# Kernel tuning notes

Hardware: AMD Instinct MI355X
Metric: run time of the kernel (lower is better)

The kernel has to match this reference:

```python
import jax, jax.numpy as jnp
import numpy as np

D, H1, O, E = 1024, 4096, 1024, 8
B = 8192


def setup_inputs() -> dict:
    key = jax.random.key(0)
    k1, k2, k3, k4 = jax.random.split(key, 4)
    # kaiming_uniform_ with nonlinearity='relu': bound = sqrt(6 / fan_in), fan_in = last dim
    b_w1 = float(np.sqrt(6.0 / D))
    b_w2 = float(np.sqrt(6.0 / H1))
    x = jax.random.normal(k1, (B, D), dtype=jnp.float32)
    eid = jax.random.randint(k2, (B,), 0, E, dtype=jnp.int32)
    W1 = jax.random.uniform(k3, (E, H1, D), dtype=jnp.float32, minval=-b_w1, maxval=b_w1)
    W2 = jax.random.uniform(k4, (E, O, H1), dtype=jnp.float32, minval=-b_w2, maxval=b_w2)
    b2 = jnp.zeros((E, O), dtype=jnp.float32)
    return {"x": x, "eid": eid, "W1": W1, "W2": W2, "b2": b2}


def reference(x, eid, W1, W2, b2):
    # Per-token expert MLP: y_i = gelu(x_i @ W1[eid_i].T) @ W2[eid_i].T + b2[eid_i]
    # Dense-dispatch formulation: loop over the (small, static) expert axis,
    # compute each expert MLP on all tokens, and select per-token via mask.
    # Math is identical to the sort/gather/scatter original.
    y = jnp.zeros((x.shape[0], W2.shape[1]), dtype=x.dtype)
    for e in range(W1.shape[0]):
        h = jax.nn.gelu(x @ W1[e].T, approximate=False)   # [B, H1]
        y_e = h @ W2[e].T + b2[e]                          # [B, O]
        mask = (eid == e)[:, None].astype(x.dtype)
        y = y + mask * y_e
    return y
```

## Files before the change

### kernel.cpp

```cpp
#include <hip/hip_runtime.h>
#include <hip/hip_bf16.h>
#include <math.h>

constexpr int kD  = 1024;
constexpr int kH1 = 4096;
constexpr int kO  = 1024;
constexpr int kE  = 8;
constexpr int kB  = 8192;

constexpr int BM = 128;
constexpr int BN = 128;
constexpr int BK = 32;
constexpr int MAXT = kB / BM + kE;

typedef __attribute__((ext_vector_type(8))) short short8;
typedef __attribute__((ext_vector_type(4))) float f32x4;

__device__ __forceinline__ unsigned short f2bf(float f) {
  unsigned int u = __float_as_uint(f);
  u += 0x7fffu + ((u >> 16) & 1u);
  return (unsigned short)(u >> 16);
}

__device__ __forceinline__ float gelu_exact(float v) {
  return 0.5f * v * (1.0f + erff(v * 0.70710678118654752f));
}

__global__ __launch_bounds__(256) void setup_kernel(const int* __restrict__ eid,
                                                    int* __restrict__ perm,
                                                    int* __restrict__ tiles) {
  __shared__ int cnt[kE];
  __shared__ int off[kE];
  __shared__ int cur[kE];
  int t = threadIdx.x;
  if (t < kE) { cnt[t] = 0; cur[t] = 0; }
  __syncthreads();
  for (int i = t; i < kB; i += 256) atomicAdd(&cnt[eid[i]], 1);
  __syncthreads();
  if (t == 0) {
    int o = 0, nt = 0;
    for (int e = 0; e < kE; ++e) {
      off[e] = o;
      int c = cnt[e];
      for (int r = 0; r < c; r += BM) {
        tiles[nt * 4 + 0] = e;
        tiles[nt * 4 + 1] = o + r;
        tiles[nt * 4 + 2] = (c - r < BM) ? (c - r) : BM;
        tiles[nt * 4 + 3] = 0;
        ++nt;
      }
      o += c;
    }
    for (; nt < MAXT; ++nt) {
      tiles[nt * 4 + 0] = 0; tiles[nt * 4 + 1] = 0;
      tiles[nt * 4 + 2] = 0; tiles[nt * 4 + 3] = 0;
    }
  }
  __syncthreads();
  for (int i = t; i < kB; i += 256) {
    int e = eid[i];
    int p = off[e] + atomicAdd(&cur[e], 1);
    perm[p] = i;
  }
}

__global__ __launch_bounds__(256) void gather_kernel(const float* __restrict__ x,
                                                     const int* __restrict__ perm,
                                                     unsigned short* __restrict__ xg) {
  int idx = blockIdx.x * 256 + threadIdx.x;
  int pos = idx >> 7;
  int c   = (idx & 127) << 3;
  int row = perm[pos];
  const float4* s = (const float4*)(x + (size_t)row * kD + c);
  float4 f0 = s[0], f1 = s[1];
  short8 v;
  v[0] = (short)f2bf(f0.x); v[1] = (short)f2bf(f0.y);
  v[2] = (short)f2bf(f0.z); v[3] = (short)f2bf(f0.w);
  v[4] = (short)f2bf(f1.x); v[5] = (short)f2bf(f1.y);
  v[6] = (short)f2bf(f1.z); v[7] = (short)f2bf(f1.w);
  *(short8*)(xg + (size_t)pos * kD + c) = v;
}

__global__ __launch_bounds__(256) void convert_kernel(const float* __restrict__ src,
                                                      unsigned short* __restrict__ dst,
                                                      int n8) {
  int stride = gridDim.x * 256;
  for (int i = blockIdx.x * 256 + threadIdx.x; i < n8; i += stride) {
    const float4* s = (const float4*)(src + (size_t)i * 8);
    float4 f0 = s[0], f1 = s[1];
    short8 v;
    v[0] = (short)f2bf(f0.x); v[1] = (short)f2bf(f0.y);
    v[2] = (short)f2bf(f0.z); v[3] = (short)f2bf(f0.w);
    v[4] = (short)f2bf(f1.x); v[5] = (short)f2bf(f1.y);
    v[6] = (short)f2bf(f1.z); v[7] = (short)f2bf(f1.w);
    *(short8*)(dst + (size_t)i * 8) = v;
  }
}

template <int K, int N, bool GELU, bool BIAS, bool OUTBF>
__global__ __launch_bounds__(256) void gemm_kernel(
    const unsigned short* __restrict__ Amat,
    const unsigned short* __restrict__ Bmat,
    const float* __restrict__ bias,
    const int* __restrict__ tiles,
    const int* __restrict__ perm,
    unsigned short* __restrict__ out_bf,
    float* __restrict__ out_f) {
  const int ti = blockIdx.x;
  const int e  = tiles[ti * 4 + 0];
  const int rs = tiles[ti * 4 + 1];
  const int nr = tiles[ti * 4 + 2];
  if (nr == 0) return;
  const int n0 = blockIdx.y * BN;

  __shared__ __align__(16) unsigned short As[2][BM * BK];
  __shared__ __align__(16) unsigned short Bs[2][BM * BK];

  const int t  = threadIdx.x;
  const int l  = t & 63;
  const int w  = t >> 6;
  const int wr = w >> 1;
  const int wc = w & 1;

  const unsigned short* Bp = Bmat + (size_t)e * N * K;

  f32x4 acc[4][4] = {};

  auto stage = [&](int buf, int k0) {
#pragma unroll
    for (int i = 0; i < 2; ++i) {
      int elem = (i * 256 + t) * 8;
      int r = elem >> 5;
      int c = elem & (BK - 1);
      const unsigned short* src = Amat + (size_t)(rs + r) * K + k0 + c;
      __builtin_amdgcn_global_load_lds(
          (const __attribute__((address_space(1))) unsigned int*)src,
          (__attribute__((address_space(3))) unsigned int*)(&As[buf][elem]),
          16, 0, 0);
    }
#pragma unroll
    for (int i = 0; i < 2; ++i) {
      int elem = (i * 256 + t) * 8;
      int r = elem >> 5;
      int c = elem & (BK - 1);
      const unsigned short* src = Bp + (size_t)(n0 + r) * K + k0 + c;
      __builtin_amdgcn_global_load_lds(
          (const __attribute__((address_space(1))) unsigned int*)src,
          (__attribute__((address_space(3))) unsigned int*)(&Bs[buf][elem]),
          16, 0, 0);
    }
  };

  stage(0, 0);
  __syncthreads();

  constexpr int NK = K / BK;
  for (int kt = 0; kt < NK; ++kt) {
    int cur = kt & 1;
    if (kt + 1 < NK) stage(cur ^ 1, (kt + 1) * BK);

    short8 a[4], b[4];
#pragma unroll
    for (int m = 0; m < 4; ++m)
      a[m] = *(const short8*)&As[cur][(wr * 64 + m * 16 + (l & 15)) * BK + (l >> 4) * 8];
#pragma unroll
    for (int n = 0; n < 4; ++n)
      b[n] = *(const short8*)&Bs[cur][(wc * 64 + n * 16 + (l & 15)) * BK + (l >> 4) * 8];

#pragma unroll
    for (int m = 0; m < 4; ++m)
#pragma unroll
      for (int n = 0; n < 4; ++n)
        acc[m][n] = __builtin_amdgcn_mfma_f32_16x16x32_bf16(a[m], b[n], acc[m][n], 0, 0, 0);

    __syncthreads();
  }

  const int lr4 = (l >> 4) * 4;
  const int lc  = l & 15;
#pragma unroll
  for (int m = 0; m < 4; ++m) {
#pragma unroll
    for (int r = 0; r < 4; ++r) {
      int row_t = wr * 64 + m * 16 + lr4 + r;
      if (row_t < nr) {
        if constexpr (OUTBF) {
          unsigned short* dst = out_bf + (size_t)(rs + row_t) * N + n0;
#pragma unroll
          for (int n = 0; n < 4; ++n) {
            float v = acc[m][n][r];
            if constexpr (GELU) v = gelu_exact(v);
            dst[wc * 64 + n * 16 + lc] = f2bf(v);
          }
        } else {
          int orig = perm[rs + row_t];
          float* dst = out_f + (size_t)orig * N + n0;
#pragma unroll
          for (int n = 0; n < 4; ++n) {
            float v = acc[m][n][r];
            if constexpr (BIAS) v += bias[(size_t)e * N + n0 + wc * 64 + n * 16 + lc];
            dst[wc * 64 + n * 16 + lc] = v;
          }
        }
      }
    }
  }
}

extern "C" void kernel_launch(void* const* d_in, const int* in_sizes, int n_in,
                              void* d_out, int out_size, void* d_ws, size_t ws_size,
                              hipStream_t stream) {
  const float* x  = (const float*)d_in[0];
  const int*  eid = (const int*)d_in[1];
  const float* W1 = (const float*)d_in[2];
  const float* W2 = (const float*)d_in[3];
  const float* b2 = (const float*)d_in[4];
  float* y = (float*)d_out;

  char* ws = (char*)d_ws;
  int* perm  = (int*)ws;
  int* tiles = (int*)(ws + 32768);
  unsigned short* xg = (unsigned short*)(ws + 36864);
  size_t xg_bytes = (size_t)(kB + BM) * kD * 2;
  unsigned short* h  = (unsigned short*)(ws + 36864 + xg_bytes);
  size_t h_bytes = (size_t)(kB + BM) * kH1 * 2;
  unsigned short* Wb = (unsigned short*)(ws + 36864 + xg_bytes + h_bytes);

  constexpr int kWelems8 = kE * kH1 * kD / 8;

  setup_kernel<<<1, 256, 0, stream>>>(eid, perm, tiles);
  gather_kernel<<<(kB * kD / 8) / 256, 256, 0, stream>>>(x, perm, xg);

  convert_kernel<<<2048, 256, 0, stream>>>(W1, Wb, kWelems8);

  gemm_kernel<kD, kH1, true, false, true>
      <<<dim3(MAXT, kH1 / BN), 256, 0, stream>>>(xg, Wb, nullptr, tiles, perm, h, nullptr);

  convert_kernel<<<2048, 256, 0, stream>>>(W2, Wb, kWelems8);

  gemm_kernel<kH1, kO, false, true, false>
      <<<dim3(MAXT, kO / BN), 256, 0, stream>>>(h, Wb, b2, tiles, perm, nullptr, y);
}
```

Measured before the change: 375.0 us.

## Rewrite grouped GEMM with 256x256 tiles, swizzled LDS and 8-wave ping-pong pipeline

Replaces the 128x128x32 GEMM with a 512-thread, 256x256x64 tile kernel that uses 128KB of dynamic LDS and XOR-swizzled layouts to avoid bank conflicts. Loads are split into quarter stages that are interleaved with MFMA quadrants, gated by explicit vmcnt waits, barriers and s_setprio, so global loads overlap compute. The grid is flattened and remapped so consecutive blocks are spread across XCDs. Larger tiles raise arithmetic intensity per LDS and global load, at the cost of more padding waste on partial expert tiles and heavy register and LDS pressure.

```diff
diff --git a/kernel.cpp b/kernel.cpp
--- a/kernel.cpp
+++ b/kernel.cpp
@@ -8,9 +8,7 @@
 constexpr int kE  = 8;
 constexpr int kB  = 8192;
 
-constexpr int BM = 128;
-constexpr int BN = 128;
-constexpr int BK = 32;
+constexpr int BM = 256;
 constexpr int MAXT = kB / BM + kE;
 
 typedef __attribute__((ext_vector_type(8))) short short8;
@@ -98,7 +96,7 @@
 }
 
 template <int K, int N, bool GELU, bool BIAS, bool OUTBF>
-__global__ __launch_bounds__(256) void gemm_kernel(
+__global__ __launch_bounds__(512, 2) void gemm8p_kernel(
     const unsigned short* __restrict__ Amat,
     const unsigned short* __restrict__ Bmat,
     const float* __restrict__ bias,
@@ -106,105 +104,176 @@
     const int* __restrict__ perm,
     unsigned short* __restrict__ out_bf,
     float* __restrict__ out_f) {
-  const int ti = blockIdx.x;
+  extern __shared__ unsigned short lds[];
+  constexpr int NKt = K / 64;
+
+  const int total = MAXT * (N / 256);
+  const int cpx = total >> 3;
+  const int bid = blockIdx.x;
+  const int id = (bid & 7) * cpx + (bid >> 3);
+  const int ti = id % MAXT;
+  const int n0 = (id / MAXT) * 256;
+
   const int e  = tiles[ti * 4 + 0];
   const int rs = tiles[ti * 4 + 1];
   const int nr = tiles[ti * 4 + 2];
   if (nr == 0) return;
-  const int n0 = blockIdx.y * BN;
-
-  __shared__ __align__(16) unsigned short As[2][BM * BK];
-  __shared__ __align__(16) unsigned short Bs[2][BM * BK];
-
-  const int t  = threadIdx.x;
-  const int l  = t & 63;
-  const int w  = t >> 6;
-  const int wr = w >> 1;
-  const int wc = w & 1;
+
+  const int t = threadIdx.x;
+  const int l = t & 63;
+  const int w = t >> 6;
+  const int r0 = (w >> 2) * 64;
+  const int c0 = (w & 3) * 32;
 
   const unsigned short* Bp = Bmat + (size_t)e * N * K;
 
-  f32x4 acc[4][4] = {};
-
-  auto stage = [&](int buf, int k0) {
+  auto ldsA = [&](int buf, int ha) { return lds + (buf * 2 + ha) * 8192; };
+  auto ldsB = [&](int buf, int hb) { return lds + 32768 + (buf * 2 + hb) * 8192; };
+
+  auto stage = [&](int H) {
+    const int slot = H & 3;
+    const int ktS = H >> 2, buf = ktS & 1, k0 = ktS * 64;
 #pragma unroll
     for (int i = 0; i < 2; ++i) {
-      int elem = (i * 256 + t) * 8;
-      int r = elem >> 5;
-      int c = elem & (BK - 1);
-      const unsigned short* src = Amat + (size_t)(rs + r) * K + k0 + c;
+      int elem = (i * 512 + t) * 8;
+      int r = elem >> 6, cp = elem & 63;
+      int cl = cp ^ ((r & 7) << 3);
+      const unsigned short* src;
+      unsigned short* dst;
+      if (slot == 0 || slot == 3) {
+        src = Amat + (size_t)(rs + (slot == 3 ? 128 : 0) + r) * K + k0 + cl;
+        dst = ldsA(buf, slot == 3 ? 1 : 0) + elem;
+      } else {
+        src = Bp + (size_t)(n0 + (slot == 2 ? 128 : 0) + r) * K + k0 + cl;
+        dst = ldsB(buf, slot == 2 ? 1 : 0) + elem;
+      }
       __builtin_amdgcn_global_load_lds(
           (const __attribute__((address_space(1))) unsigned int*)src,
-          (__attribute__((address_space(3))) unsigned int*)(&As[buf][elem]),
-          16, 0, 0);
-    }
-#pragma unroll
-    for (int i = 0; i < 2; ++i) {
-      int elem = (i * 256 + t) * 8;
-      int r = elem >> 5;
-      int c = elem & (BK - 1);
-      const unsigned short* src = Bp + (size_t)(n0 + r) * K + k0 + c;
-      __builtin_amdgcn_global_load_lds(
-          (const __attribute__((address_space(1))) unsigned int*)src,
-          (__attribute__((address_space(3))) unsigned int*)(&Bs[buf][elem]),
-          16, 0, 0);
+          (__attribute__((address_space(3))) unsigned int*)dst, 16, 0, 0);
     }
   };
 
-  stage(0, 0);
-  __syncthreads();
-
-  constexpr int NK = K / BK;
-  for (int kt = 0; kt < NK; ++kt) {
-    int cur = kt & 1;
-    if (kt + 1 < NK) stage(cur ^ 1, (kt + 1) * BK);
-
-    short8 a[4], b[4];
-#pragma unroll
-    for (int m = 0; m < 4; ++m)
-      a[m] = *(const short8*)&As[cur][(wr * 64 + m * 16 + (l & 15)) * BK + (l >> 4) * 8];
-#pragma unroll
-    for (int n = 0; n < 4; ++n)
-      b[n] = *(const short8*)&Bs[cur][(wc * 64 + n * 16 + (l & 15)) * BK + (l >> 4) * 8];
-
-#pragma unroll
-    for (int m = 0; m < 4; ++m)
-#pragma unroll
-      for (int n = 0; n < 4; ++n)
-        acc[m][n] = __builtin_amdgcn_mfma_f32_16x16x32_bf16(a[m], b[n], acc[m][n], 0, 0, 0);
-
-    __syncthreads();
+  short8 aF[4][2], bF0[2][2], bF1[2][2];
+  f32x4 acc[2][2][4][2] = {};
+
+  auto loadA = [&](int buf, int ha) {
+#pragma unroll
+    for (int mr = 0; mr < 4; ++mr)
+#pragma unroll
+      for (int ks = 0; ks < 2; ++ks) {
+        int r = r0 + mr * 16 + (l & 15);
+        int c = (ks * 32 + (l >> 4) * 8) ^ ((r & 7) << 3);
+        aF[mr][ks] = *(const short8*)(ldsA(buf, ha) + r * 64 + c);
+      }
+  };
+  auto loadB = [&](int buf, int hb, short8 (*bF)[2]) {
+#pragma unroll
+    for (int nc = 0; nc < 2; ++nc)
+#pragma unroll
+      for (int ks = 0; ks < 2; ++ks) {
+        int r = c0 + nc * 16 + (l & 15);
+        int c = (ks * 32 + (l >> 4) * 8) ^ ((r & 7) << 3);
+        bF[nc][ks] = *(const short8*)(ldsB(buf, hb) + r * 64 + c);
+      }
+  };
+  auto mfmaQ = [&](int qr, int qc, short8 (*bF)[2]) {
+    __builtin_amdgcn_s_setprio(1);
+#pragma unroll
+    for (int mr = 0; mr < 4; ++mr)
+#pragma unroll
+      for (int nc = 0; nc < 2; ++nc)
+#pragma unroll
+        for (int ks = 0; ks < 2; ++ks)
+          acc[qr][qc][mr][nc] = __builtin_amdgcn_mfma_f32_16x16x32_bf16(
+              aF[mr][ks], bF[nc][ks], acc[qr][qc][mr][nc], 0, 0, 0);
+    __builtin_amdgcn_s_setprio(0);
+  };
+
+#pragma unroll
+  for (int H = 0; H < 4; ++H) stage(H);
+  asm volatile("s_waitcnt vmcnt(4)" ::: "memory");
+#pragma unroll
+  for (int H = 4; H < 7; ++H) stage(H);
+
+  for (int kt = 0; kt < NKt - 1; ++kt) {
+    const int buf = kt & 1;
+    asm volatile("s_waitcnt vmcnt(6)" ::: "memory");
+    __builtin_amdgcn_s_barrier();
+    loadA(buf, 0);
+    loadB(buf, 0, bF0);
+    { int H = 4 * kt + 7;  if (H < 4 * NKt) stage(H); }
+    __builtin_amdgcn_s_barrier();
+    mfmaQ(0, 0, bF0);
+    __builtin_amdgcn_s_barrier();
+    loadB(buf, 1, bF1);
+    { int H = 4 * kt + 8;  if (H < 4 * NKt) stage(H); }
+    __builtin_amdgcn_s_barrier();
+    mfmaQ(0, 1, bF1);
+    __builtin_amdgcn_s_barrier();
+    loadA(buf, 1);
+    { int H = 4 * kt + 9;  if (H < 4 * NKt) stage(H); }
+    __builtin_amdgcn_s_barrier();
+    mfmaQ(1, 0, bF0);
+    __builtin_amdgcn_s_barrier();
+    { int H = 4 * kt + 10; if (H < 4 * NKt) stage(H); }
+    __builtin_amdgcn_s_barrier();
+    mfmaQ(1, 1, bF1);
+  }
+  {
+    const int buf = (NKt - 1) & 1;
+    asm volatile("s_waitcnt vmcnt(0)" ::: "memory");
+    __builtin_amdgcn_s_barrier();
+    loadA(buf, 0);
+    loadB(buf, 0, bF0);
+    __builtin_amdgcn_s_barrier();
+    mfmaQ(0, 0, bF0);
+    __builtin_amdgcn_s_barrier();
+    loadB(buf, 1, bF1);
+    __builtin_amdgcn_s_barrier();
+    mfmaQ(0, 1, bF1);
+    __builtin_amdgcn_s_barrier();
+    loadA(buf, 1);
+    __builtin_amdgcn_s_barrier();
+    mfmaQ(1, 0, bF0);
+    __builtin_amdgcn_s_barrier();
+    mfmaQ(1, 1, bF1);
   }
 
   const int lr4 = (l >> 4) * 4;
   const int lc  = l & 15;
 #pragma unroll
-  for (int m = 0; m < 4; ++m) {
-#pragma unroll
-    for (int r = 0; r < 4; ++r) {
-      int row_t = wr * 64 + m * 16 + lr4 + r;
-      if (row_t < nr) {
-        if constexpr (OUTBF) {
-          unsigned short* dst = out_bf + (size_t)(rs + row_t) * N + n0;
-#pragma unroll
-          for (int n = 0; n < 4; ++n) {
-            float v = acc[m][n][r];
-            if constexpr (GELU) v = gelu_exact(v);
-            dst[wc * 64 + n * 16 + lc] = f2bf(v);
-          }
-        } else {
-          int orig = perm[rs + row_t];
-          float* dst = out_f + (size_t)orig * N + n0;
-#pragma unroll
-          for (int n = 0; n < 4; ++n) {
-            float v = acc[m][n][r];
-            if constexpr (BIAS) v += bias[(size_t)e * N + n0 + wc * 64 + n * 16 + lc];
-            dst[wc * 64 + n * 16 + lc] = v;
+  for (int qr = 0; qr < 2; ++qr)
+#pragma unroll
+    for (int mr = 0; mr < 4; ++mr)
+#pragma unroll
+      for (int rg = 0; rg < 4; ++rg) {
+        int row = qr * 128 + r0 + mr * 16 + lr4 + rg;
+        if (row < nr) {
+          if constexpr (OUTBF) {
+            unsigned short* dst = out_bf + (size_t)(rs + row) * N + n0;
+#pragma unroll
+            for (int qc = 0; qc < 2; ++qc)
+#pragma unroll
+              for (int nc = 0; nc < 2; ++nc) {
+                float v = acc[qr][qc][mr][nc][rg];
+                if constexpr (GELU) v = gelu_exact(v);
+                dst[qc * 128 + c0 + nc * 16 + lc] = f2bf(v);
+              }
+          } else {
+            int orig = perm[rs + row];
+            float* dst = out_f + (size_t)orig * N + n0;
+#pragma unroll
+            for (int qc = 0; qc < 2; ++qc)
+#pragma unroll
+              for (int nc = 0; nc < 2; ++nc) {
+                float v = acc[qr][qc][mr][nc][rg];
+                if constexpr (BIAS)
+                  v += bias[(size_t)e * N + n0 + qc * 128 + c0 + nc * 16 + lc];
+                dst[qc * 128 + c0 + nc * 16 + lc] = v;
+              }
           }
         }
       }
-    }
-  }
 }
 
 extern "C" void kernel_launch(void* const* d_in, const int* in_sizes, int n_in,
@@ -228,16 +297,17 @@
 
   constexpr int kWelems8 = kE * kH1 * kD / 8;
 
+  auto g1 = gemm8p_kernel<kD, kH1, true, false, true>;
+  auto g2 = gemm8p_kernel<kH1, kO, false, true, false>;
+  hipFuncSetAttribute((const void*)g1, hipFuncAttributeMaxDynamicSharedMemorySize, 131072);
+  hipFuncSetAttribute((const void*)g2, hipFuncAttributeMaxDynamicSharedMemorySize, 131072);
+
   setup_kernel<<<1, 256, 0, stream>>>(eid, perm, tiles);
   gather_kernel<<<(kB * kD / 8) / 256, 256, 0, stream>>>(x, perm, xg);
 
   convert_kernel<<<2048, 256, 0, stream>>>(W1, Wb, kWelems8);
-
-  gemm_kernel<kD, kH1, true, false, true>
-      <<<dim3(MAXT, kH1 / BN), 256, 0, stream>>>(xg, Wb, nullptr, tiles, perm, h, nullptr);
+  g1<<<MAXT * (kH1 / 256), 512, 131072, stream>>>(xg, Wb, nullptr, tiles, perm, h, nullptr);
 
   convert_kernel<<<2048, 256, 0, stream>>>(W2, Wb, kWelems8);
-
-  gemm_kernel<kH1, kO, false, true, false>
-      <<<dim3(MAXT, kO / BN), 256, 0, stream>>>(h, Wb, b2, tiles, perm, nullptr, y);
-}
+  g2<<<MAXT * (kO / 256), 512, 131072, stream>>>(h, Wb, b2, tiles, perm, nullptr, y);
+}
```

Measured after the change: 333.2 us. 11.1% less time.
